# Optimization experiments

Hardware: AMD Instinct MI355X
Metric: run time of the kernel (lower is better)

## Reference

```python
import jax, jax.numpy as jnp
import numpy as np

B, S, D, H = 2, 2048, 1024, 16
HD = D // H


def setup_inputs() -> dict:
    key = jax.random.key(0)
    ks = jax.random.split(key, 9)
    s = 1.0 / np.sqrt(D)
    return {
        "qx": jax.random.normal(ks[0], (B, S, D), jnp.float32),
        "kx": jax.random.normal(ks[1], (B, S, D), jnp.float32),
        "vx": jax.random.normal(ks[2], (B, S, D), jnp.float32),
        "mask": jnp.tril(jnp.ones((S, S), jnp.int32))[None, None],  # [1,1,S,S] causal
        "Wq": jax.random.uniform(ks[3], (D, D), jnp.float32, -s, s),
        "bq": jax.random.uniform(ks[4], (D,), jnp.float32, -s, s),
        "Wk": jax.random.uniform(ks[5], (D, D), jnp.float32, -s, s),
        "bk": jax.random.uniform(ks[6], (D,), jnp.float32, -s, s),
        "Wv": jax.random.uniform(ks[7], (D, D), jnp.float32, -s, s),
        "bv": jax.random.uniform(ks[8], (D,), jnp.float32, -s, s),
    }


def reference(qx, kx, vx, mask, Wq, bq, Wk, bk, Wv, bv):
    bat, seq_len, d_model = qx.shape
    # torch Linear: y = x @ W.T + b
    q = qx @ Wq.T + bq
    k = kx @ Wk.T + bk
    v = vx @ Wv.T + bv
    # [b, h, s, hd]
    q = q.reshape(bat, seq_len, H, HD).transpose(0, 2, 1, 3)
    k = k.reshape(bat, seq_len, H, HD).transpose(0, 2, 1, 3)
    v = v.reshape(bat, seq_len, H, HD).transpose(0, 2, 1, 3)
    # NOTE: original scales by sqrt(d_model), not sqrt(head_dim)
    attn_weight = jnp.einsum('bhqd,bhkd->bhqk', q, k) / jnp.sqrt(
        jnp.asarray(d_model, q.dtype))
    attn_weight = jnp.where(mask == 0, -jnp.inf, attn_weight)
    attn_score = jax.nn.softmax(attn_weight, axis=-1)
    attn_output = jnp.einsum('bhqk,bhkd->bhqd', attn_score, v)
    return attn_output.transpose(0, 2, 1, 3).reshape(bat, seq_len, d_model)
```

## Files before the change

kernel.cpp:

```cpp
#include <hip/hip_runtime.h>


typedef __attribute__((ext_vector_type(8))) short short8;
typedef __attribute__((ext_vector_type(4))) short shortx4;
typedef __attribute__((ext_vector_type(4))) float floatx4;

#define NEGBIG (-1.0e30f)
#define QSCALE 0.04508422002778011f

__device__ __forceinline__ float bf2f(ushort u) {
    union { unsigned int i; float f; } x; x.i = ((unsigned int)u) << 16; return x.f;
}
__device__ __forceinline__ ushort f2bf(float f) {
    union { unsigned int i; float f; } x; x.f = f;
    return (ushort)((x.i + 0x7FFFu + ((x.i >> 16) & 1u)) >> 16);
}
__device__ __forceinline__ ushort f2bf_trunc(float f) {
    union { unsigned int i; float f; } x; x.f = f;
    return (ushort)(x.i >> 16);
}
__device__ __forceinline__ void gl_lds16(const void* g, void* l) {
    __builtin_amdgcn_global_load_lds(
        (const __attribute__((address_space(1))) unsigned int*)g,
        (__attribute__((address_space(3))) unsigned int*)l, 16, 0, 0);
}

__global__ void detect_dtype(const unsigned int* __restrict__ w, int* __restrict__ flag) {
    const int lane = threadIdx.x;
    int hits = 0;
    for (int i = 0; i < 16; ++i) {
        unsigned int v = w[lane * 16 + i];
        int e = (int)((v >> 7) & 0xFF);
        hits += (e >= 100 && e <= 135) ? 1 : 0;
    }
    for (int off = 32; off; off >>= 1) hits += __shfl_down(hits, off);
    if (lane == 0) *flag = (hits > 512) ? 1 : 0;
}

__global__ void convert_fp32(
    const float* __restrict__ qx, const float* __restrict__ kx, const float* __restrict__ vx,
    const float* __restrict__ wq, const float* __restrict__ wk, const float* __restrict__ wv,
    const float* __restrict__ bq, const float* __restrict__ bk, const float* __restrict__ bv,
    ushort* __restrict__ dst, const int* __restrict__ flag)
{
    if (*flag) return;
    const int v = blockIdx.x * 256 + threadIdx.x;
    const float* src; int off = v;
    if      (v < 1048576) { src = qx; }
    else if (v < 2097152) { src = kx; off = v - 1048576; }
    else if (v < 3145728) { src = vx; off = v - 2097152; }
    else if (v < 3407872) { src = wq; off = v - 3145728; }
    else if (v < 3670016) { src = wk; off = v - 3407872; }
    else if (v < 3932160) { src = wv; off = v - 3670016; }
    else if (v < 3932416) { src = bq; off = v - 3932160; }
    else if (v < 3932672) { src = bk; off = v - 3932416; }
    else                  { src = bv; off = v - 3932672; }
    float4 f = ((const float4*)src)[off];
    shortx4 o;
    o[0] = (short)f2bf(f.x); o[1] = (short)f2bf(f.y);
    o[2] = (short)f2bf(f.z); o[3] = (short)f2bf(f.w);
    *(shortx4*)&dst[(size_t)v * 4] = o;
}

__global__ __launch_bounds__(256, 4) void qkv_gemm(
    const void* __restrict__ Xq_, const void* __restrict__ Wq_, const void* __restrict__ bq_,
    const void* __restrict__ Xk_, const void* __restrict__ Wk_, const void* __restrict__ bk_,
    const void* __restrict__ Xv_, const void* __restrict__ Wv_, const void* __restrict__ bv_,
    const ushort* __restrict__ conv,
    ushort* __restrict__ Yq, ushort* __restrict__ Yk, ushort* __restrict__ Yv,
    const int* __restrict__ flag)
{
    const int idx = blockIdx.x;
    const int xcd = idx & 7;
    const int j   = (idx >> 3) & 7;
    const int pg  = idx >> 6;
    const int p   = pg * 8 + xcd;
    const int z   = p >> 5;
    const int m0  = (p & 31) * 128;
    const int n0  = j * 128;

    const int dt = *flag;
    const ushort* X = dt ? (const ushort*)(z == 0 ? Xq_ : z == 1 ? Xk_ : Xv_)
                         : conv + (size_t)z * 4194304;
    const ushort* W = dt ? (const ushort*)(z == 0 ? Wq_ : z == 1 ? Wk_ : Wv_)
                         : conv + 12582912 + (size_t)z * 1048576;
    const ushort* bias = dt ? (const ushort*)(z == 0 ? bq_ : z == 1 ? bk_ : bv_)
                            : conv + 15728640 + z * 1024;
    ushort* Y = (z == 0) ? Yq : (z == 1) ? Yk : Yv;
    const float oscale = (z == 0) ? QSCALE : 1.0f;

    __shared__ __align__(16) ushort As[128 * 64];
    __shared__ __align__(16) ushort Bs[128 * 64];

    const int tid  = threadIdx.x;
    const int wave = tid >> 6;
    const int lane = tid & 63;
    const int col  = lane & 15;
    const int quad = lane >> 4;
    const int wm   = (wave >> 1) * 64;
    const int wn   = (wave & 1) * 64;

    floatx4 acc[4][4] = {};

    for (int k0 = 0; k0 < 1024; k0 += 64) {
        __syncthreads();
#pragma unroll
        for (int c = 0; c < 4; ++c) {
            const int o   = c * 4096 + tid * 16;
            const int row = o >> 7;
            const int bg  = ((o >> 4) & 7) ^ (row & 7);
            gl_lds16(X + (size_t)(m0 + row) * 1024 + k0 + bg * 8, &As[o >> 1]);
            gl_lds16(W + (size_t)(n0 + row) * 1024 + k0 + bg * 8, &Bs[o >> 1]);
        }
        __syncthreads();

#pragma unroll
        for (int h = 0; h < 2; ++h) {
            short8 af[4], bf_[4];
#pragma unroll
            for (int i = 0; i < 4; ++i) {
                const int ra = wm + i * 16 + col;
                const int rb = wn + i * 16 + col;
                af[i]  = *(const short8*)&As[ra * 64 + (((h * 4 + quad) ^ (ra & 7)) * 8)];
                bf_[i] = *(const short8*)&Bs[rb * 64 + (((h * 4 + quad) ^ (rb & 7)) * 8)];
            }
#pragma unroll
            for (int i = 0; i < 4; ++i)
#pragma unroll
                for (int jj = 0; jj < 4; ++jj)
                    acc[i][jj] = __builtin_amdgcn_mfma_f32_16x16x32_bf16(af[i], bf_[jj], acc[i][jj], 0, 0, 0);
        }
    }

    if (z == 2) {
#pragma unroll
        for (int jj = 0; jj < 4; ++jj) {
            const int n = n0 + wn + jj * 16 + col;
            const float bb = bf2f(bias[n]);
#pragma unroll
            for (int i = 0; i < 4; ++i) {
                const int m = m0 + wm + i * 16 + quad * 4;
                shortx4 pk;
#pragma unroll
                for (int r = 0; r < 4; ++r) pk[r] = (short)f2bf(acc[i][jj][r] + bb);
                *(shortx4*)&Y[((size_t)(m >> 11) * 1024 + n) * 2048 + (m & 2047)] = pk;
            }
        }
    } else {
#pragma unroll
        for (int jj = 0; jj < 4; ++jj) {
            const int n = n0 + wn + jj * 16 + col;
            const float bb = bf2f(bias[n]);
#pragma unroll
            for (int i = 0; i < 4; ++i)
#pragma unroll
                for (int r = 0; r < 4; ++r) {
                    const int m = m0 + wm + i * 16 + quad * 4 + r;
                    Y[(size_t)m * 1024 + n] = f2bf((acc[i][jj][r] + bb) * oscale);
                }
        }
    }
}

#define LDP 72

__global__ __launch_bounds__(256, 4) void attn(
    const ushort* __restrict__ Q, const ushort* __restrict__ K,
    const ushort* __restrict__ Vt, void* __restrict__ O,
    const int* __restrict__ flag)
{
    const int idx = blockIdx.x;
    const int bx  = (idx >> 3) & 15;
    const int g   = (idx >> 7) * 8 + (idx & 7);
    const int b   = g >> 4;
    const int h   = g & 15;
    const int dt  = *flag;

    __shared__ __align__(16) ushort Qs[64 * 64];
    __shared__ __align__(16) ushort Ks[2][64 * 64];
    __shared__ __align__(16) ushort Vs[2][64 * 64];
    __shared__ __align__(16) ushort Ps[4][16 * LDP];

    const int tid  = threadIdx.x;
    const int wave = tid >> 6;
    const int lane = tid & 63;
    const int col  = lane & 15;
    const int quad = lane >> 4;

    const size_t qkbase = ((size_t)b * 2048) * 1024 + h * 64;
    const size_t vtbase = ((size_t)(b * 16 + h) * 64) * 2048;

    short8 ones;
#pragma unroll
    for (int i = 0; i < 8; ++i) ones[i] = (short)0x3F80;

    const int o0   = tid * 16;
    const int o1   = 4096 + tid * 16;
    const int row0 = o0 >> 7, row1 = o1 >> 7;
    const int bg0  = ((o0 >> 4) & 7) ^ (row0 & 7);
    const int bg1  = ((o1 >> 4) & 7) ^ (row1 & 7);

    for (int seg = 0; seg < 2; ++seg) {
        const int qt = seg ? (31 - bx) : bx;
        const int q0 = qt * 64;

        __syncthreads();
        gl_lds16(Q + qkbase + (size_t)(q0 + row0) * 1024 + bg0 * 8, &Qs[o0 >> 1]);
        gl_lds16(Q + qkbase + (size_t)(q0 + row1) * 1024 + bg1 * 8, &Qs[o1 >> 1]);
        gl_lds16(K + qkbase + (size_t)row0 * 1024 + bg0 * 8, &Ks[0][o0 >> 1]);
        gl_lds16(K + qkbase + (size_t)row1 * 1024 + bg1 * 8, &Ks[0][o1 >> 1]);
        gl_lds16(Vt + vtbase + (size_t)row0 * 2048 + bg0 * 8, &Vs[0][o0 >> 1]);
        gl_lds16(Vt + vtbase + (size_t)row1 * 2048 + bg1 * 8, &Vs[0][o1 >> 1]);
        __syncthreads();

        const int rq = wave * 16 + col;
        const short8 qf0 = *(const short8*)&Qs[rq * 64 + (((quad    ) ^ (col & 7)) * 8)];
        const short8 qf1 = *(const short8*)&Qs[rq * 64 + (((quad + 4) ^ (col & 7)) * 8)];

        floatx4 oacc[4] = {};
        floatx4 sacc = {};

        for (int t = 0; t <= qt; ++t) {
            const int cur = t & 1;

            if (t < qt) {
                const int kv1 = (t + 1) * 64;
                const int nb  = cur ^ 1;
                gl_lds16(K + qkbase + (size_t)(kv1 + row0) * 1024 + bg0 * 8, &Ks[nb][o0 >> 1]);
                gl_lds16(K + qkbase + (size_t)(kv1 + row1) * 1024 + bg1 * 8, &Ks[nb][o1 >> 1]);
                gl_lds16(Vt + vtbase + (size_t)row0 * 2048 + kv1 + bg0 * 8, &Vs[nb][o0 >> 1]);
                gl_lds16(Vt + vtbase + (size_t)row1 * 2048 + kv1 + bg1 * 8, &Vs[nb][o1 >> 1]);
            }

            floatx4 s4[4];
#pragma unroll
            for (int ct = 0; ct < 4; ++ct) {
                const int rk = ct * 16 + col;
                short8 kf0 = *(const short8*)&Ks[cur][rk * 64 + (((quad    ) ^ (col & 7)) * 8)];
                short8 kf1 = *(const short8*)&Ks[cur][rk * 64 + (((quad + 4) ^ (col & 7)) * 8)];
                floatx4 a = {};
                a = __builtin_amdgcn_mfma_f32_16x16x32_bf16(qf0, kf0, a, 0, 0, 0);
                a = __builtin_amdgcn_mfma_f32_16x16x32_bf16(qf1, kf1, a, 0, 0, 0);
                s4[ct] = a;
            }

            if (t == qt) {
#pragma unroll
                for (int ct = 0; ct < 4; ++ct) {
                    const int kidx = ct * 16 + col;
#pragma unroll
                    for (int r = 0; r < 4; ++r) {
                        const int qidx = wave * 16 + quad * 4 + r;
                        s4[ct][r] = (kidx <= qidx) ? s4[ct][r] : NEGBIG;
                    }
                }
            }

#pragma unroll
            for (int ct = 0; ct < 4; ++ct)
#pragma unroll
                for (int r = 0; r < 4; ++r) {
                    float pv = __builtin_exp2f(s4[ct][r]);
                    Ps[wave][(quad * 4 + r) * LDP + ct * 16 + col] = f2bf_trunc(pv);
                }

            short8 pf0 = *(const short8*)&Ps[wave][col * LDP + quad * 8];
            short8 pf1 = *(const short8*)&Ps[wave][col * LDP + 32 + quad * 8];

            sacc = __builtin_amdgcn_mfma_f32_16x16x32_bf16(pf0, ones, sacc, 0, 0, 0);
            sacc = __builtin_amdgcn_mfma_f32_16x16x32_bf16(pf1, ones, sacc, 0, 0, 0);

#pragma unroll
            for (int ct = 0; ct < 4; ++ct) {
                const int rv = ct * 16 + col;
                short8 vf0 = *(const short8*)&Vs[cur][rv * 64 + (((quad    ) ^ (rv & 7)) * 8)];
                short8 vf1 = *(const short8*)&Vs[cur][rv * 64 + (((quad + 4) ^ (rv & 7)) * 8)];
                oacc[ct] = __builtin_amdgcn_mfma_f32_16x16x32_bf16(pf0, vf0, oacc[ct], 0, 0, 0);
                oacc[ct] = __builtin_amdgcn_mfma_f32_16x16x32_bf16(pf1, vf1, oacc[ct], 0, 0, 0);
            }

            __syncthreads();
        }

#pragma unroll
        for (int r = 0; r < 4; ++r) {
            const float inv = 1.0f / sacc[r];
            const int q = q0 + wave * 16 + quad * 4 + r;
#pragma unroll
            for (int ct = 0; ct < 4; ++ct) {
                const float v = oacc[ct][r] * inv;
                const size_t oidx = ((size_t)b * 2048 + q) * 1024 + h * 64 + ct * 16 + col;
                if (dt) ((ushort*)O)[oidx] = f2bf(v);
                else    ((float*)O)[oidx]  = v;
            }
        }
    }
}

extern "C" void kernel_launch(void* const* d_in, const int* in_sizes, int n_in,
                              void* d_out, int out_size, void* d_ws, size_t ws_size,
                              hipStream_t stream) {
    const void* qx = d_in[0];
    const void* kx = d_in[1];
    const void* vx = d_in[2];
    const void* Wq = d_in[4]; const void* bq = d_in[5];
    const void* Wk = d_in[6]; const void* bk = d_in[7];
    const void* Wv = d_in[8]; const void* bv = d_in[9];

    int*    flag = (int*)d_ws;
    ushort* conv = (ushort*)((char*)d_ws + 256);
    ushort* Qw   = (ushort*)((char*)d_ws + 256 + 31463424);
    ushort* Kw   = Qw + (size_t)4096 * 1024;
    ushort* Vtw  = Kw + (size_t)4096 * 1024;

    detect_dtype<<<1, 64, 0, stream>>>((const unsigned int*)qx, flag);

    convert_fp32<<<15363, 256, 0, stream>>>(
        (const float*)qx, (const float*)kx, (const float*)vx,
        (const float*)Wq, (const float*)Wk, (const float*)Wv,
        (const float*)bq, (const float*)bk, (const float*)bv, conv, flag);

    qkv_gemm<<<768, 256, 0, stream>>>(qx, Wq, bq, kx, Wk, bk, vx, Wv, bv,
                                      conv, Qw, Kw, Vtw, flag);

    attn<<<512, 256, 0, stream>>>(Qw, Kw, Vtw, d_out, flag);
}
```

Before: 205.2 us.

## Split attention into one q-tile per block, single-buffer KV, fold dtype detect

The dtype-detection kernel is removed and its logic folded into every convert_fp32 block, which saves one launch at the cost of each block re-reading a small header of qx. The attention kernel no longer pairs q-tiles bx and 31-bx inside one block. It launches 1024 blocks, each handling one q-tile, ordered from the heaviest tiles first and mapped across XCDs. K/V staging drops from double to single buffering, which halves LDS use to allow more resident blocks but puts the global load latency back on the critical path, with two barriers per step.

```diff
diff --git a/kernel.cpp b/kernel.cpp
--- a/kernel.cpp
+++ b/kernel.cpp
@@ -25,25 +25,28 @@
         (__attribute__((address_space(3))) unsigned int*)l, 16, 0, 0);
 }
 
-__global__ void detect_dtype(const unsigned int* __restrict__ w, int* __restrict__ flag) {
-    const int lane = threadIdx.x;
-    int hits = 0;
-    for (int i = 0; i < 16; ++i) {
-        unsigned int v = w[lane * 16 + i];
-        int e = (int)((v >> 7) & 0xFF);
-        hits += (e >= 100 && e <= 135) ? 1 : 0;
-    }
-    for (int off = 32; off; off >>= 1) hits += __shfl_down(hits, off);
-    if (lane == 0) *flag = (hits > 512) ? 1 : 0;
-}
-
 __global__ void convert_fp32(
     const float* __restrict__ qx, const float* __restrict__ kx, const float* __restrict__ vx,
     const float* __restrict__ wq, const float* __restrict__ wk, const float* __restrict__ wv,
     const float* __restrict__ bq, const float* __restrict__ bk, const float* __restrict__ bv,
-    ushort* __restrict__ dst, const int* __restrict__ flag)
+    ushort* __restrict__ dst, int* __restrict__ flag)
 {
-    if (*flag) return;
+    const unsigned int* w = (const unsigned int*)qx;
+    int hits = 0;
+#pragma unroll
+    for (int i = 0; i < 4; ++i) {
+        unsigned int v = w[threadIdx.x * 4 + i];
+        int e = (int)((v >> 7) & 0xFF);
+        hits += (e >= 100 && e <= 135) ? 1 : 0;
+    }
+    __shared__ int red[4];
+    for (int off = 32; off; off >>= 1) hits += __shfl_down(hits, off);
+    if ((threadIdx.x & 63) == 0) red[threadIdx.x >> 6] = hits;
+    __syncthreads();
+    const int dt = (red[0] + red[1] + red[2] + red[3] > 512) ? 1 : 0;
+    if (blockIdx.x == 0 && threadIdx.x == 0) *flag = dt;
+    if (dt) return;
+
     const int v = blockIdx.x * 256 + threadIdx.x;
     const float* src; int off = v;
     if      (v < 1048576) { src = qx; }
@@ -169,16 +172,19 @@
     const ushort* __restrict__ Vt, void* __restrict__ O,
     const int* __restrict__ flag)
 {
-    const int idx = blockIdx.x;
-    const int bx  = (idx >> 3) & 15;
-    const int g   = (idx >> 7) * 8 + (idx & 7);
+    const int i   = blockIdx.x;
+    const int xcd = i & 7;
+    const int i3  = i >> 3;
+    const int qt  = 31 - (i3 & 31);
+    const int g   = xcd + 8 * (i3 >> 5);
     const int b   = g >> 4;
     const int h   = g & 15;
+    const int q0  = qt * 64;
     const int dt  = *flag;
 
     __shared__ __align__(16) ushort Qs[64 * 64];
-    __shared__ __align__(16) ushort Ks[2][64 * 64];
-    __shared__ __align__(16) ushort Vs[2][64 * 64];
+    __shared__ __align__(16) ushort Ks[64 * 64];
+    __shared__ __align__(16) ushort Vs[64 * 64];
     __shared__ __align__(16) ushort Ps[4][16 * LDP];
 
     const int tid  = threadIdx.x;
@@ -192,7 +198,7 @@
 
     short8 ones;
 #pragma unroll
-    for (int i = 0; i < 8; ++i) ones[i] = (short)0x3F80;
+    for (int ii = 0; ii < 8; ++ii) ones[ii] = (short)0x3F80;
 
     const int o0   = tid * 16;
     const int o1   = 4096 + tid * 16;
@@ -200,99 +206,90 @@
     const int bg0  = ((o0 >> 4) & 7) ^ (row0 & 7);
     const int bg1  = ((o1 >> 4) & 7) ^ (row1 & 7);
 
-    for (int seg = 0; seg < 2; ++seg) {
-        const int qt = seg ? (31 - bx) : bx;
-        const int q0 = qt * 64;
-
-        __syncthreads();
-        gl_lds16(Q + qkbase + (size_t)(q0 + row0) * 1024 + bg0 * 8, &Qs[o0 >> 1]);
-        gl_lds16(Q + qkbase + (size_t)(q0 + row1) * 1024 + bg1 * 8, &Qs[o1 >> 1]);
-        gl_lds16(K + qkbase + (size_t)row0 * 1024 + bg0 * 8, &Ks[0][o0 >> 1]);
-        gl_lds16(K + qkbase + (size_t)row1 * 1024 + bg1 * 8, &Ks[0][o1 >> 1]);
-        gl_lds16(Vt + vtbase + (size_t)row0 * 2048 + bg0 * 8, &Vs[0][o0 >> 1]);
-        gl_lds16(Vt + vtbase + (size_t)row1 * 2048 + bg1 * 8, &Vs[0][o1 >> 1]);
-        __syncthreads();
-
-        const int rq = wave * 16 + col;
-        const short8 qf0 = *(const short8*)&Qs[rq * 64 + (((quad    ) ^ (col & 7)) * 8)];
-        const short8 qf1 = *(const short8*)&Qs[rq * 64 + (((quad + 4) ^ (col & 7)) * 8)];
-
-        floatx4 oacc[4] = {};
-        floatx4 sacc = {};
-
-        for (int t = 0; t <= qt; ++t) {
-            const int cur = t & 1;
-
-            if (t < qt) {
-                const int kv1 = (t + 1) * 64;
-                const int nb  = cur ^ 1;
-                gl_lds16(K + qkbase + (size_t)(kv1 + row0) * 1024 + bg0 * 8, &Ks[nb][o0 >> 1]);
-                gl_lds16(K + qkbase + (size_t)(kv1 + row1) * 1024 + bg1 * 8, &Ks[nb][o1 >> 1]);
-                gl_lds16(Vt + vtbase + (size_t)row0 * 2048 + kv1 + bg0 * 8, &Vs[nb][o0 >> 1]);
-                gl_lds16(Vt + vtbase + (size_t)row1 * 2048 + kv1 + bg1 * 8, &Vs[nb][o1 >> 1]);
-            }
-
-            floatx4 s4[4];
+    gl_lds16(Q + qkbase + (size_t)(q0 + row0) * 1024 + bg0 * 8, &Qs[o0 >> 1]);
+    gl_lds16(Q + qkbase + (size_t)(q0 + row1) * 1024 + bg1 * 8, &Qs[o1 >> 1]);
+    gl_lds16(K + qkbase + (size_t)row0 * 1024 + bg0 * 8, &Ks[o0 >> 1]);
+    gl_lds16(K + qkbase + (size_t)row1 * 1024 + bg1 * 8, &Ks[o1 >> 1]);
+    gl_lds16(Vt + vtbase + (size_t)row0 * 2048 + bg0 * 8, &Vs[o0 >> 1]);
+    gl_lds16(Vt + vtbase + (size_t)row1 * 2048 + bg1 * 8, &Vs[o1 >> 1]);
+    __syncthreads();
+
+    const int rq = wave * 16 + col;
+    const short8 qf0 = *(const short8*)&Qs[rq * 64 + (((quad    ) ^ (col & 7)) * 8)];
+    const short8 qf1 = *(const short8*)&Qs[rq * 64 + (((quad + 4) ^ (col & 7)) * 8)];
+
+    floatx4 oacc[4] = {};
+    floatx4 sacc = {};
+
+    for (int t = 0; t <= qt; ++t) {
+        floatx4 s4[4];
+#pragma unroll
+        for (int ct = 0; ct < 4; ++ct) {
+            const int rk = ct * 16 + col;
+            short8 kf0 = *(const short8*)&Ks[rk * 64 + (((quad    ) ^ (col & 7)) * 8)];
+            short8 kf1 = *(const short8*)&Ks[rk * 64 + (((quad + 4) ^ (col & 7)) * 8)];
+            floatx4 a = {};
+            a = __builtin_amdgcn_mfma_f32_16x16x32_bf16(qf0, kf0, a, 0, 0, 0);
+            a = __builtin_amdgcn_mfma_f32_16x16x32_bf16(qf1, kf1, a, 0, 0, 0);
+            s4[ct] = a;
+        }
+
+        if (t == qt) {
 #pragma unroll
             for (int ct = 0; ct < 4; ++ct) {
-                const int rk = ct * 16 + col;
-                short8 kf0 = *(const short8*)&Ks[cur][rk * 64 + (((quad    ) ^ (col & 7)) * 8)];
-                short8 kf1 = *(const short8*)&Ks[cur][rk * 64 + (((quad + 4) ^ (col & 7)) * 8)];
-                floatx4 a = {};
-                a = __builtin_amdgcn_mfma_f32_16x16x32_bf16(qf0, kf0, a, 0, 0, 0);
-                a = __builtin_amdgcn_mfma_f32_16x16x32_bf16(qf1, kf1, a, 0, 0, 0);
-                s4[ct] = a;
-            }
-
-            if (t == qt) {
-#pragma unroll
-                for (int ct = 0; ct < 4; ++ct) {
-                    const int kidx = ct * 16 + col;
-#pragma unroll
-                    for (int r = 0; r < 4; ++r) {
-                        const int qidx = wave * 16 + quad * 4 + r;
-                        s4[ct][r] = (kidx <= qidx) ? s4[ct][r] : NEGBIG;
-                    }
+                const int kidx = ct * 16 + col;
+#pragma unroll
+                for (int r = 0; r < 4; ++r) {
+                    const int qidx = wave * 16 + quad * 4 + r;
+                    s4[ct][r] = (kidx <= qidx) ? s4[ct][r] : NEGBIG;
                 }
             }
-
-#pragma unroll
-            for (int ct = 0; ct < 4; ++ct)
-#pragma unroll
-                for (int r = 0; r < 4; ++r) {
-                    float pv = __builtin_exp2f(s4[ct][r]);
-                    Ps[wave][(quad * 4 + r) * LDP + ct * 16 + col] = f2bf_trunc(pv);
-                }
-
-            short8 pf0 = *(const short8*)&Ps[wave][col * LDP + quad * 8];
-            short8 pf1 = *(const short8*)&Ps[wave][col * LDP + 32 + quad * 8];
-
-            sacc = __builtin_amdgcn_mfma_f32_16x16x32_bf16(pf0, ones, sacc, 0, 0, 0);
-            sacc = __builtin_amdgcn_mfma_f32_16x16x32_bf16(pf1, ones, sacc, 0, 0, 0);
-
-#pragma unroll
-            for (int ct = 0; ct < 4; ++ct) {
-                const int rv = ct * 16 + col;
-                short8 vf0 = *(const short8*)&Vs[cur][rv * 64 + (((quad    ) ^ (rv & 7)) * 8)];
-                short8 vf1 = *(const short8*)&Vs[cur][rv * 64 + (((quad + 4) ^ (rv & 7)) * 8)];
-                oacc[ct] = __builtin_amdgcn_mfma_f32_16x16x32_bf16(pf0, vf0, oacc[ct], 0, 0, 0);
-                oacc[ct] = __builtin_amdgcn_mfma_f32_16x16x32_bf16(pf1, vf1, oacc[ct], 0, 0, 0);
+        }
+
+#pragma unroll
+        for (int ct = 0; ct < 4; ++ct)
+#pragma unroll
+            for (int r = 0; r < 4; ++r) {
+                float pv = __builtin_exp2f(s4[ct][r]);
+                Ps[wave][(quad * 4 + r) * LDP + ct * 16 + col] = f2bf_trunc(pv);
             }
 
+        short8 pf0 = *(const short8*)&Ps[wave][col * LDP + quad * 8];
+        short8 pf1 = *(const short8*)&Ps[wave][col * LDP + 32 + quad * 8];
+
+        sacc = __builtin_amdgcn_mfma_f32_16x16x32_bf16(pf0, ones, sacc, 0, 0, 0);
+        sacc = __builtin_amdgcn_mfma_f32_16x16x32_bf16(pf1, ones, sacc, 0, 0, 0);
+
+#pragma unroll
+        for (int ct = 0; ct < 4; ++ct) {
+            const int rv = ct * 16 + col;
+            short8 vf0 = *(const short8*)&Vs[rv * 64 + (((quad    ) ^ (rv & 7)) * 8)];
+            short8 vf1 = *(const short8*)&Vs[rv * 64 + (((quad + 4) ^ (rv & 7)) * 8)];
+            oacc[ct] = __builtin_amdgcn_mfma_f32_16x16x32_bf16(pf0, vf0, oacc[ct], 0, 0, 0);
+            oacc[ct] = __builtin_amdgcn_mfma_f32_16x16x32_bf16(pf1, vf1, oacc[ct], 0, 0, 0);
+        }
+
+        if (t < qt) {
+            const int kv1 = (t + 1) * 64;
             __syncthreads();
-        }
-
-#pragma unroll
-        for (int r = 0; r < 4; ++r) {
-            const float inv = 1.0f / sacc[r];
-            const int q = q0 + wave * 16 + quad * 4 + r;
-#pragma unroll
-            for (int ct = 0; ct < 4; ++ct) {
-                const float v = oacc[ct][r] * inv;
-                const size_t oidx = ((size_t)b * 2048 + q) * 1024 + h * 64 + ct * 16 + col;
-                if (dt) ((ushort*)O)[oidx] = f2bf(v);
-                else    ((float*)O)[oidx]  = v;
-            }
+            gl_lds16(K + qkbase + (size_t)(kv1 + row0) * 1024 + bg0 * 8, &Ks[o0 >> 1]);
+            gl_lds16(K + qkbase + (size_t)(kv1 + row1) * 1024 + bg1 * 8, &Ks[o1 >> 1]);
+            gl_lds16(Vt + vtbase + (size_t)row0 * 2048 + kv1 + bg0 * 8, &Vs[o0 >> 1]);
+            gl_lds16(Vt + vtbase + (size_t)row1 * 2048 + kv1 + bg1 * 8, &Vs[o1 >> 1]);
+            __syncthreads();
+        }
+    }
+
+#pragma unroll
+    for (int r = 0; r < 4; ++r) {
+        const float inv = 1.0f / sacc[r];
+        const int q = q0 + wave * 16 + quad * 4 + r;
+#pragma unroll
+        for (int ct = 0; ct < 4; ++ct) {
+            const float v = oacc[ct][r] * inv;
+            const size_t oidx = ((size_t)b * 2048 + q) * 1024 + h * 64 + ct * 16 + col;
+            if (dt) ((ushort*)O)[oidx] = f2bf(v);
+            else    ((float*)O)[oidx]  = v;
         }
     }
 }
@@ -313,8 +310,6 @@
     ushort* Kw   = Qw + (size_t)4096 * 1024;
     ushort* Vtw  = Kw + (size_t)4096 * 1024;
 
-    detect_dtype<<<1, 64, 0, stream>>>((const unsigned int*)qx, flag);
-
     convert_fp32<<<15363, 256, 0, stream>>>(
         (const float*)qx, (const float*)kx, (const float*)vx,
         (const float*)Wq, (const float*)Wk, (const float*)Wv,
@@ -323,5 +318,5 @@
     qkv_gemm<<<768, 256, 0, stream>>>(qx, Wq, bq, kx, Wk, bk, vx, Wv, bv,
                                       conv, Qw, Kw, Vtw, flag);
 
-    attn<<<512, 256, 0, stream>>>(Qw, Kw, Vtw, d_out, flag);
-}
+    attn<<<1024, 256, 0, stream>>>(Qw, Kw, Vtw, d_out, flag);
+}
```

Result: slower. 218.0 us (+6.3%).
